# Performance work log

Hardware: AMD Instinct MI355X
Metric: run time of the kernel (lower is better)

Reference implementation:

```python
import jax, jax.numpy as jnp
import numpy as np

DIM = 128
N_HEADS = 4
HEAD_DIM = DIM // N_HEADS
K = 16
B, N = 2, 8192
BIAS_HID = 32


def knn_idx(xyz, k):
    # squared pairwise distances: [B,N,N] (same argsort order as cdist)
    sq = jnp.sum(xyz * xyz, axis=-1)  # [B,N]
    d2 = sq[:, :, None] + sq[:, None, :] - 2.0 * jnp.einsum('bnd,bmd->bnm', xyz, xyz)
    _, idx = jax.lax.top_k(-d2, k)  # smallest distances
    return idx  # [B,N,k]


def setup_inputs() -> dict:
    key = jax.random.key(0)
    ks = jax.random.split(key, 12)
    s = 1.0 / np.sqrt(DIM)
    inp = {
        'x':   jax.random.normal(ks[0], (B, N, DIM), jnp.float32),
        'xyz': jax.random.normal(ks[1], (B, N, 3), jnp.float32),
        'Wq': jax.random.uniform(ks[2], (DIM, DIM), jnp.float32, -s, s),
        'bq': jnp.zeros((DIM,), jnp.float32),
        'Wk': jax.random.uniform(ks[3], (DIM, DIM), jnp.float32, -s, s),
        'bk': jnp.zeros((DIM,), jnp.float32),
        'Wv': jax.random.uniform(ks[4], (DIM, DIM), jnp.float32, -s, s),
        'bv': jnp.zeros((DIM,), jnp.float32),
        'Wo': jax.random.uniform(ks[5], (DIM, DIM), jnp.float32, -s, s),
        'bo': jnp.zeros((DIM,), jnp.float32),
        'W1': jax.random.uniform(ks[6], (3, BIAS_HID), jnp.float32, -0.5, 0.5),
        'b1': jnp.zeros((BIAS_HID,), jnp.float32),
        'W2': jax.random.uniform(ks[7], (BIAS_HID, N_HEADS), jnp.float32, -1.0 / np.sqrt(BIAS_HID), 1.0 / np.sqrt(BIAS_HID)),
        'b2': jnp.zeros((N_HEADS,), jnp.float32),
    }
    return inp


def reference(x, xyz, Wq, bq, Wk, bk, Wv, bv, Wo, bo, W1, b1, W2, b2):
    Bb, Nn, C = x.shape
    idx = knn_idx(xyz, K)  # [B,N,k]

    q = (x @ Wq + bq).reshape(Bb, Nn, N_HEADS, HEAD_DIM)
    kf = (x @ Wk + bk).reshape(Bb, Nn, N_HEADS, HEAD_DIM)
    vf = (x @ Wv + bv).reshape(Bb, Nn, N_HEADS, HEAD_DIM)

    gather = jax.vmap(lambda f, i: f[i])  # per-batch fancy gather
    kn = gather(kf, idx)  # [B,N,k,H,D]
    vn = gather(vf, idx)  # [B,N,k,H,D]
    nxyz = gather(xyz, idx)  # [B,N,k,3]

    rel = xyz[:, :, None, :] - nxyz  # [B,N,k,3]
    bias = jax.nn.relu(rel @ W1 + b1) @ W2 + b2  # [B,N,k,H]

    scores = jnp.einsum('bnhd,bnkhd->bnhk', q, kn) / np.sqrt(HEAD_DIM)
    scores = scores + jnp.swapaxes(bias, 2, 3)  # [B,N,H,k]
    attn = jax.nn.softmax(scores, axis=-1)
    out = jnp.einsum('bnhk,bnkhd->bnhd', attn, vn).reshape(Bb, Nn, C)
    return out @ Wo + bo
```

## Files before the change

kernel.cpp:

```cpp
#include <hip/hip_runtime.h>
#include <hip/hip_bf16.h>
#include <math.h>

#define BATCH 2
#define NPT   8192
#define DIMC  128
#define NH    4
#define KNN_K 16
#define HID   32
#define BN    (BATCH*NPT)

#define TILE 1024
#define QPW  2
#define NWV  4

__device__ __forceinline__ float readlane_f(float v, int l) {
  return __int_as_float(__builtin_amdgcn_readlane(__float_as_int(v), l));
}

__global__ __launch_bounds__(256) void knn_kernel(const float* __restrict__ xyz,
                                                  int* __restrict__ knn_out) {
  __shared__ float4 spts[TILE];
  const int tid  = threadIdx.x;
  const int lane = tid & 63;
  const int wave = tid >> 6;
  const int qbase = blockIdx.x * (NWV*QPW) + wave * QPW;
  const int b = qbase / NPT;

  float qx[QPW], qy[QPW], qz[QPW], qsq[QPW];
  float topd[QPW]; int topi[QPW]; float tau[QPW];
#pragma unroll
  for (int qi = 0; qi < QPW; ++qi) {
    const int g = qbase + qi;
    qx[qi] = xyz[(size_t)g*3+0];
    qy[qi] = xyz[(size_t)g*3+1];
    qz[qi] = xyz[(size_t)g*3+2];
    qsq[qi] = __fadd_rn(__fadd_rn(__fmul_rn(qx[qi],qx[qi]),
                                  __fmul_rn(qy[qi],qy[qi])),
                        __fmul_rn(qz[qi],qz[qi]));
    topd[qi] = 3e38f; topi[qi] = 0; tau[qi] = 3e38f;
  }

  for (int t = 0; t < NPT/TILE; ++t) {
    __syncthreads();
    const float* src = xyz + (size_t)(b*NPT + t*TILE)*3;
    for (int i = tid; i < TILE; i += 256) {
      const float x = src[i*3+0], y = src[i*3+1], z = src[i*3+2];
      const float sq = __fadd_rn(__fadd_rn(__fmul_rn(x,x), __fmul_rn(y,y)),
                                 __fmul_rn(z,z));
      spts[i] = make_float4(x+x, y+y, z+z, sq);
    }
    __syncthreads();

    for (int c = 0; c < TILE/64; ++c) {
      const float4 cd = spts[c*64 + lane];
      const int cbase = t*TILE + c*64;
#pragma unroll
      for (int qi = 0; qi < QPW; ++qi) {
        float dot2 = __fadd_rn(__fadd_rn(__fmul_rn(qx[qi],cd.x),
                                         __fmul_rn(qy[qi],cd.y)),
                               __fmul_rn(qz[qi],cd.z));
        float d2 = __fsub_rn(__fadd_rn(qsq[qi], cd.w), dot2);
        unsigned long long m = __ballot(d2 < tau[qi]);
        while (m) {
          const int l = (int)__builtin_ctzll(m);
          const float dn = readlane_f(d2, l);
          const int   ni_ = cbase + l;
          const float my  = topd[qi];
          const int   myi = topi[qi];
          float ab  = __shfl_up(my, 1);
          int   abi = __shfl_up(myi, 1);
          if (lane == 0) ab = -3e38f;
          const bool ge = dn < my;
          const bool gt = dn < ab;
          topd[qi] = ge ? (gt ? ab  : dn ) : my;
          topi[qi] = ge ? (gt ? abi : ni_) : myi;
          tau[qi] = readlane_f(topd[qi], 15);
          m &= (m - 1);
          if (m) m &= __ballot(d2 < tau[qi]);
        }
      }
    }
  }

#pragma unroll
  for (int qi = 0; qi < QPW; ++qi) {
    if (lane < KNN_K) knn_out[(size_t)(qbase + qi)*KNN_K + lane] = topi[qi];
  }
}

__device__ __forceinline__ float f4c(const float4 v, int u) {
  return u == 0 ? v.x : u == 1 ? v.y : u == 2 ? v.z : v.w;
}

__global__ __launch_bounds__(256) void qkv_kernel(const float* __restrict__ x,
    const float* __restrict__ Wq, const float* __restrict__ bq,
    const float* __restrict__ Wk, const float* __restrict__ bk,
    const float* __restrict__ Wv, const float* __restrict__ bv,
    float* __restrict__ q, float* __restrict__ k, float* __restrict__ v) {
  __shared__ float xs[16*DIMC];
  const int tid = threadIdx.x;
  const int rowbase = blockIdx.x * 16;
  {
    float4* xs4 = (float4*)xs;
    const float4* src4 = (const float4*)(x + (size_t)rowbase*DIMC);
    for (int i = tid; i < 16*DIMC/4; i += 256) xs4[i] = src4[i];
  }
  __syncthreads();

  const int cg = tid & 31, rg = tid >> 5;
  const int c0 = cg * 4;
  float4 aq0 = *(const float4*)&bq[c0], aq1 = aq0;
  float4 ak0 = *(const float4*)&bk[c0], ak1 = ak0;
  float4 av0 = *(const float4*)&bv[c0], av1 = av0;

  for (int kk = 0; kk < DIMC; kk += 4) {
    const float4 xa = *(const float4*)&xs[rg*DIMC + kk];
    const float4 xb = *(const float4*)&xs[(rg+8)*DIMC + kk];
#pragma unroll
    for (int u = 0; u < 4; ++u) {
      const float4 wq = *(const float4*)&Wq[(size_t)(kk+u)*DIMC + c0];
      const float4 wk = *(const float4*)&Wk[(size_t)(kk+u)*DIMC + c0];
      const float4 wv = *(const float4*)&Wv[(size_t)(kk+u)*DIMC + c0];
      const float xau = f4c(xa, u), xbu = f4c(xb, u);
      aq0.x = fmaf(xau, wq.x, aq0.x); aq0.y = fmaf(xau, wq.y, aq0.y);
      aq0.z = fmaf(xau, wq.z, aq0.z); aq0.w = fmaf(xau, wq.w, aq0.w);
      aq1.x = fmaf(xbu, wq.x, aq1.x); aq1.y = fmaf(xbu, wq.y, aq1.y);
      aq1.z = fmaf(xbu, wq.z, aq1.z); aq1.w = fmaf(xbu, wq.w, aq1.w);
      ak0.x = fmaf(xau, wk.x, ak0.x); ak0.y = fmaf(xau, wk.y, ak0.y);
      ak0.z = fmaf(xau, wk.z, ak0.z); ak0.w = fmaf(xau, wk.w, ak0.w);
      ak1.x = fmaf(xbu, wk.x, ak1.x); ak1.y = fmaf(xbu, wk.y, ak1.y);
      ak1.z = fmaf(xbu, wk.z, ak1.z); ak1.w = fmaf(xbu, wk.w, ak1.w);
      av0.x = fmaf(xau, wv.x, av0.x); av0.y = fmaf(xau, wv.y, av0.y);
      av0.z = fmaf(xau, wv.z, av0.z); av0.w = fmaf(xau, wv.w, av0.w);
      av1.x = fmaf(xbu, wv.x, av1.x); av1.y = fmaf(xbu, wv.y, av1.y);
      av1.z = fmaf(xbu, wv.z, av1.z); av1.w = fmaf(xbu, wv.w, av1.w);
    }
  }

  const size_t r0 = (size_t)(rowbase + rg)*DIMC + c0;
  const size_t r1 = (size_t)(rowbase + rg + 8)*DIMC + c0;
  *(float4*)&q[r0] = aq0; *(float4*)&q[r1] = aq1;
  *(float4*)&k[r0] = ak0; *(float4*)&k[r1] = ak1;
  *(float4*)&v[r0] = av0; *(float4*)&v[r1] = av1;
}

template <int CTRL>
__device__ __forceinline__ float dppf(float x) {
  return __int_as_float(__builtin_amdgcn_update_dpp(
      __float_as_int(x), __float_as_int(x), CTRL, 0xF, 0xF, false));
}
#define ROR1 0x121
#define ROR2 0x122
#define ROR4 0x124
#define ROR8 0x128

__global__ __launch_bounds__(256) void attn_kernel(const float* __restrict__ xyz,
    const int* __restrict__ knn, const float* __restrict__ qb,
    const float* __restrict__ kb, const float* __restrict__ vb,
    const float* __restrict__ W1, const float* __restrict__ b1,
    const float* __restrict__ W2, const float* __restrict__ b2,
    float* __restrict__ ao) {
  __shared__ float sw[4][NH][KNN_K];
  __shared__ int   sn[4][KNN_K];
  const int tid  = threadIdx.x;
  const int wave = tid >> 6;
  const int lane = tid & 63;
  const int p = blockIdx.x * 4 + wave;
  const int b = p / NPT;
  const int h = lane >> 4;
  const int j = lane & 15;

  const int nj = knn[(size_t)p*KNN_K + j];
  if (h == 0) sn[wave][j] = nj;
  const size_t nn = (size_t)b*NPT + nj;

  const float qx0 = xyz[(size_t)p*3+0];
  const float qy0 = xyz[(size_t)p*3+1];
  const float qz0 = xyz[(size_t)p*3+2];
  const float rx = qx0 - xyz[nn*3+0];
  const float ry = qy0 - xyz[nn*3+1];
  const float rz = qz0 - xyz[nn*3+2];
  float bias = b2[h];
#pragma unroll 8
  for (int u = 0; u < HID; ++u) {
    float hv = rx*W1[0*HID+u] + ry*W1[1*HID+u] + rz*W1[2*HID+u] + b1[u];
    hv = hv > 0.f ? hv : 0.f;
    bias = fmaf(hv, W2[u*NH + h], bias);
  }

  const float* qrow = qb + (size_t)p*DIMC + h*32;
  const float* krow = kb + nn*DIMC + h*32;
  float s = 0.f;
#pragma unroll
  for (int u = 0; u < 32; u += 4) {
    const float4 qv = *(const float4*)(qrow + u);
    const float4 kv = *(const float4*)(krow + u);
    s = fmaf(qv.x, kv.x, s); s = fmaf(qv.y, kv.y, s);
    s = fmaf(qv.z, kv.z, s); s = fmaf(qv.w, kv.w, s);
  }
  s = s * 0.17677669529663689f + bias;

  float m = s;
  m = fmaxf(m, dppf<ROR1>(m));
  m = fmaxf(m, dppf<ROR2>(m));
  m = fmaxf(m, dppf<ROR4>(m));
  m = fmaxf(m, dppf<ROR8>(m));
  const float e = expf(s - m);
  float ssum = e;
  ssum += dppf<ROR1>(ssum);
  ssum += dppf<ROR2>(ssum);
  ssum += dppf<ROR4>(ssum);
  ssum += dppf<ROR8>(ssum);
  sw[wave][h][j] = e / ssum;

  __syncthreads();

  const int d0 = lane;
  const int hA = d0 >> 5;
  float out0 = 0.f, out1 = 0.f;
  const float* vbase = vb + (size_t)b*NPT*DIMC;
#pragma unroll 4
  for (int j2 = 0; j2 < KNN_K; ++j2) {
    const int n = sn[wave][j2];
    const float wA = sw[wave][hA][j2];
    const float wB = sw[wave][2+hA][j2];
    const float* vrow = vbase + (size_t)n*DIMC;
    out0 = fmaf(wA, vrow[d0],    out0);
    out1 = fmaf(wB, vrow[64+d0], out1);
  }
  ao[(size_t)p*DIMC + d0]      = out0;
  ao[(size_t)p*DIMC + 64 + d0] = out1;
}

__global__ __launch_bounds__(256) void proj_kernel(float* __restrict__ inout,
    const float* __restrict__ Wo, const float* __restrict__ bo) {
  __shared__ float xs[16*DIMC];
  const int tid = threadIdx.x;
  const int rowbase = blockIdx.x * 16;
  {
    float4* xs4 = (float4*)xs;
    const float4* src4 = (const float4*)(inout + (size_t)rowbase*DIMC);
    for (int i = tid; i < 16*DIMC/4; i += 256) xs4[i] = src4[i];
  }
  __syncthreads();

  const int cg = tid & 31, rg = tid >> 5;
  const int c0 = cg * 4;
  float4 a0 = *(const float4*)&bo[c0], a1 = a0;

  for (int kk = 0; kk < DIMC; kk += 4) {
    const float4 xa = *(const float4*)&xs[rg*DIMC + kk];
    const float4 xb = *(const float4*)&xs[(rg+8)*DIMC + kk];
#pragma unroll
    for (int u = 0; u < 4; ++u) {
      const float4 w = *(const float4*)&Wo[(size_t)(kk+u)*DIMC + c0];
      const float xau = f4c(xa, u), xbu = f4c(xb, u);
      a0.x = fmaf(xau, w.x, a0.x); a0.y = fmaf(xau, w.y, a0.y);
      a0.z = fmaf(xau, w.z, a0.z); a0.w = fmaf(xau, w.w, a0.w);
      a1.x = fmaf(xbu, w.x, a1.x); a1.y = fmaf(xbu, w.y, a1.y);
      a1.z = fmaf(xbu, w.z, a1.z); a1.w = fmaf(xbu, w.w, a1.w);
    }
  }

  *(float4*)&inout[(size_t)(rowbase + rg)*DIMC + c0]     = a0;
  *(float4*)&inout[(size_t)(rowbase + rg + 8)*DIMC + c0] = a1;
}

extern "C" void kernel_launch(void* const* d_in, const int* in_sizes, int n_in,
                              void* d_out, int out_size, void* d_ws, size_t ws_size,
                              hipStream_t stream) {
  const float* x   = (const float*)d_in[0];
  const float* xyz = (const float*)d_in[1];
  const float* Wq  = (const float*)d_in[2];
  const float* bq  = (const float*)d_in[3];
  const float* Wk  = (const float*)d_in[4];
  const float* bk  = (const float*)d_in[5];
  const float* Wv  = (const float*)d_in[6];
  const float* bv  = (const float*)d_in[7];
  const float* Wo  = (const float*)d_in[8];
  const float* bo  = (const float*)d_in[9];
  const float* W1  = (const float*)d_in[10];
  const float* b1  = (const float*)d_in[11];
  const float* W2  = (const float*)d_in[12];
  const float* b2  = (const float*)d_in[13];
  float* out = (float*)d_out;

  char* ws = (char*)d_ws;
  int*   knn = (int*)ws;
  float* q   = (float*)(ws + (size_t)(1u<<20));
  float* k   = (float*)(ws + (size_t)9*(1u<<20));
  float* v   = (float*)(ws + (size_t)17*(1u<<20));

  hipLaunchKernelGGL(knn_kernel, dim3(BN/(NWV*QPW)), dim3(256), 0, stream, xyz, knn);
  hipLaunchKernelGGL(qkv_kernel, dim3(BN/16), dim3(256), 0, stream,
                     x, Wq, bq, Wk, bk, Wv, bv, q, k, v);
  hipLaunchKernelGGL(attn_kernel, dim3(BN/4), dim3(256), 0, stream,
                     xyz, knn, q, k, v, W1, b1, W2, b2, out);
  hipLaunchKernelGGL(proj_kernel, dim3(BN/16), dim3(256), 0, stream,
                     out, Wo, bo);
}
```

Before: 206.4 us.

## Merge KNN and QKV kernels into one interleaved launch, tweak projection tiling

```diff
diff --git a/kernel.cpp b/kernel.cpp
--- a/kernel.cpp
+++ b/kernel.cpp
@@ -13,136 +13,148 @@
 #define TILE 1024
 #define QPW  2
 #define NWV  4
+#define KNNB (BN/(NWV*QPW))
+#define QKVB (BN/16)
 
 __device__ __forceinline__ float readlane_f(float v, int l) {
   return __int_as_float(__builtin_amdgcn_readlane(__float_as_int(v), l));
 }
-
-__global__ __launch_bounds__(256) void knn_kernel(const float* __restrict__ xyz,
-                                                  int* __restrict__ knn_out) {
-  __shared__ float4 spts[TILE];
-  const int tid  = threadIdx.x;
-  const int lane = tid & 63;
-  const int wave = tid >> 6;
-  const int qbase = blockIdx.x * (NWV*QPW) + wave * QPW;
-  const int b = qbase / NPT;
-
-  float qx[QPW], qy[QPW], qz[QPW], qsq[QPW];
-  float topd[QPW]; int topi[QPW]; float tau[QPW];
-#pragma unroll
-  for (int qi = 0; qi < QPW; ++qi) {
-    const int g = qbase + qi;
-    qx[qi] = xyz[(size_t)g*3+0];
-    qy[qi] = xyz[(size_t)g*3+1];
-    qz[qi] = xyz[(size_t)g*3+2];
-    qsq[qi] = __fadd_rn(__fadd_rn(__fmul_rn(qx[qi],qx[qi]),
-                                  __fmul_rn(qy[qi],qy[qi])),
-                        __fmul_rn(qz[qi],qz[qi]));
-    topd[qi] = 3e38f; topi[qi] = 0; tau[qi] = 3e38f;
-  }
-
-  for (int t = 0; t < NPT/TILE; ++t) {
-    __syncthreads();
-    const float* src = xyz + (size_t)(b*NPT + t*TILE)*3;
-    for (int i = tid; i < TILE; i += 256) {
-      const float x = src[i*3+0], y = src[i*3+1], z = src[i*3+2];
-      const float sq = __fadd_rn(__fadd_rn(__fmul_rn(x,x), __fmul_rn(y,y)),
-                                 __fmul_rn(z,z));
-      spts[i] = make_float4(x+x, y+y, z+z, sq);
-    }
-    __syncthreads();
-
-    for (int c = 0; c < TILE/64; ++c) {
-      const float4 cd = spts[c*64 + lane];
-      const int cbase = t*TILE + c*64;
-#pragma unroll
-      for (int qi = 0; qi < QPW; ++qi) {
-        float dot2 = __fadd_rn(__fadd_rn(__fmul_rn(qx[qi],cd.x),
-                                         __fmul_rn(qy[qi],cd.y)),
-                               __fmul_rn(qz[qi],cd.z));
-        float d2 = __fsub_rn(__fadd_rn(qsq[qi], cd.w), dot2);
-        unsigned long long m = __ballot(d2 < tau[qi]);
-        while (m) {
-          const int l = (int)__builtin_ctzll(m);
-          const float dn = readlane_f(d2, l);
-          const int   ni_ = cbase + l;
-          const float my  = topd[qi];
-          const int   myi = topi[qi];
-          float ab  = __shfl_up(my, 1);
-          int   abi = __shfl_up(myi, 1);
-          if (lane == 0) ab = -3e38f;
-          const bool ge = dn < my;
-          const bool gt = dn < ab;
-          topd[qi] = ge ? (gt ? ab  : dn ) : my;
-          topi[qi] = ge ? (gt ? abi : ni_) : myi;
-          tau[qi] = readlane_f(topd[qi], 15);
-          m &= (m - 1);
-          if (m) m &= __ballot(d2 < tau[qi]);
-        }
-      }
-    }
-  }
-
-#pragma unroll
-  for (int qi = 0; qi < QPW; ++qi) {
-    if (lane < KNN_K) knn_out[(size_t)(qbase + qi)*KNN_K + lane] = topi[qi];
-  }
-}
-
+__device__ __forceinline__ float dpp_shr1_f(float x) {
+  return __int_as_float(__builtin_amdgcn_update_dpp(
+      __float_as_int(x), __float_as_int(x), 0x111, 0xF, 0xF, false));
+}
+__device__ __forceinline__ int dpp_shr1_i(int x) {
+  return __builtin_amdgcn_update_dpp(x, x, 0x111, 0xF, 0xF, false);
+}
 __device__ __forceinline__ float f4c(const float4 v, int u) {
   return u == 0 ? v.x : u == 1 ? v.y : u == 2 ? v.z : v.w;
 }
 
-__global__ __launch_bounds__(256) void qkv_kernel(const float* __restrict__ x,
+__global__ __launch_bounds__(256) void knnqkv_kernel(
+    const float* __restrict__ xyz, int* __restrict__ knn_out,
+    const float* __restrict__ x,
     const float* __restrict__ Wq, const float* __restrict__ bq,
     const float* __restrict__ Wk, const float* __restrict__ bk,
     const float* __restrict__ Wv, const float* __restrict__ bv,
     float* __restrict__ q, float* __restrict__ k, float* __restrict__ v) {
-  __shared__ float xs[16*DIMC];
+  __shared__ float4 sbuf[TILE];
+  const int g   = blockIdx.x;
   const int tid = threadIdx.x;
-  const int rowbase = blockIdx.x * 16;
-  {
-    float4* xs4 = (float4*)xs;
-    const float4* src4 = (const float4*)(x + (size_t)rowbase*DIMC);
-    for (int i = tid; i < 16*DIMC/4; i += 256) xs4[i] = src4[i];
-  }
-  __syncthreads();
-
-  const int cg = tid & 31, rg = tid >> 5;
-  const int c0 = cg * 4;
-  float4 aq0 = *(const float4*)&bq[c0], aq1 = aq0;
-  float4 ak0 = *(const float4*)&bk[c0], ak1 = ak0;
-  float4 av0 = *(const float4*)&bv[c0], av1 = av0;
-
-  for (int kk = 0; kk < DIMC; kk += 4) {
-    const float4 xa = *(const float4*)&xs[rg*DIMC + kk];
-    const float4 xb = *(const float4*)&xs[(rg+8)*DIMC + kk];
-#pragma unroll
-    for (int u = 0; u < 4; ++u) {
-      const float4 wq = *(const float4*)&Wq[(size_t)(kk+u)*DIMC + c0];
-      const float4 wk = *(const float4*)&Wk[(size_t)(kk+u)*DIMC + c0];
-      const float4 wv = *(const float4*)&Wv[(size_t)(kk+u)*DIMC + c0];
-      const float xau = f4c(xa, u), xbu = f4c(xb, u);
-      aq0.x = fmaf(xau, wq.x, aq0.x); aq0.y = fmaf(xau, wq.y, aq0.y);
-      aq0.z = fmaf(xau, wq.z, aq0.z); aq0.w = fmaf(xau, wq.w, aq0.w);
-      aq1.x = fmaf(xbu, wq.x, aq1.x); aq1.y = fmaf(xbu, wq.y, aq1.y);
-      aq1.z = fmaf(xbu, wq.z, aq1.z); aq1.w = fmaf(xbu, wq.w, aq1.w);
-      ak0.x = fmaf(xau, wk.x, ak0.x); ak0.y = fmaf(xau, wk.y, ak0.y);
-      ak0.z = fmaf(xau, wk.z, ak0.z); ak0.w = fmaf(xau, wk.w, ak0.w);
-      ak1.x = fmaf(xbu, wk.x, ak1.x); ak1.y = fmaf(xbu, wk.y, ak1.y);
-      ak1.z = fmaf(xbu, wk.z, ak1.z); ak1.w = fmaf(xbu, wk.w, ak1.w);
-      av0.x = fmaf(xau, wv.x, av0.x); av0.y = fmaf(xau, wv.y, av0.y);
-      av0.z = fmaf(xau, wv.z, av0.z); av0.w = fmaf(xau, wv.w, av0.w);
-      av1.x = fmaf(xbu, wv.x, av1.x); av1.y = fmaf(xbu, wv.y, av1.y);
-      av1.z = fmaf(xbu, wv.z, av1.z); av1.w = fmaf(xbu, wv.w, av1.w);
-    }
-  }
-
-  const size_t r0 = (size_t)(rowbase + rg)*DIMC + c0;
-  const size_t r1 = (size_t)(rowbase + rg + 8)*DIMC + c0;
-  *(float4*)&q[r0] = aq0; *(float4*)&q[r1] = aq1;
-  *(float4*)&k[r0] = ak0; *(float4*)&k[r1] = ak1;
-  *(float4*)&v[r0] = av0; *(float4*)&v[r1] = av1;
+
+  if (g % 3 != 2) {
+    const int kb_  = (g/3)*2 + (g%3);
+    const int lane = tid & 63;
+    const int wave = tid >> 6;
+    const int qbase = kb_ * (NWV*QPW) + wave * QPW;
+    const int b = qbase / NPT;
+
+    float qx[QPW], qy[QPW], qz[QPW], qsq[QPW];
+    float topd[QPW]; int topi[QPW]; float tau[QPW];
+#pragma unroll
+    for (int qi = 0; qi < QPW; ++qi) {
+      const int gg = qbase + qi;
+      qx[qi] = xyz[(size_t)gg*3+0];
+      qy[qi] = xyz[(size_t)gg*3+1];
+      qz[qi] = xyz[(size_t)gg*3+2];
+      qsq[qi] = __fadd_rn(__fadd_rn(__fmul_rn(qx[qi],qx[qi]),
+                                    __fmul_rn(qy[qi],qy[qi])),
+                          __fmul_rn(qz[qi],qz[qi]));
+      topd[qi] = 3e38f; topi[qi] = 0; tau[qi] = 3e38f;
+    }
+
+    for (int t = 0; t < NPT/TILE; ++t) {
+      __syncthreads();
+      const float* src = xyz + (size_t)(b*NPT + t*TILE)*3;
+      for (int i = tid; i < TILE; i += 256) {
+        const float xx = src[i*3+0], yy = src[i*3+1], zz = src[i*3+2];
+        const float sq = __fadd_rn(__fadd_rn(__fmul_rn(xx,xx), __fmul_rn(yy,yy)),
+                                   __fmul_rn(zz,zz));
+        sbuf[i] = make_float4(xx+xx, yy+yy, zz+zz, sq);
+      }
+      __syncthreads();
+
+      for (int c = 0; c < TILE/64; ++c) {
+        const float4 cd = sbuf[c*64 + lane];
+        const int cbase = t*TILE + c*64;
+#pragma unroll
+        for (int qi = 0; qi < QPW; ++qi) {
+          float dot2 = __fadd_rn(__fadd_rn(__fmul_rn(qx[qi],cd.x),
+                                           __fmul_rn(qy[qi],cd.y)),
+                                 __fmul_rn(qz[qi],cd.z));
+          float d2 = __fsub_rn(__fadd_rn(qsq[qi], cd.w), dot2);
+          unsigned long long m = __ballot(d2 < tau[qi]);
+          while (m) {
+            const int l = (int)__builtin_ctzll(m);
+            const float dn = readlane_f(d2, l);
+            const int   ni_ = cbase + l;
+            const float my  = topd[qi];
+            const int   myi = topi[qi];
+            float ab  = dpp_shr1_f(my);
+            int   abi = dpp_shr1_i(myi);
+            if (lane == 0) ab = -3e38f;
+            const bool ge = dn < my;
+            const bool gt = dn < ab;
+            topd[qi] = ge ? (gt ? ab  : dn ) : my;
+            topi[qi] = ge ? (gt ? abi : ni_) : myi;
+            tau[qi] = readlane_f(topd[qi], 15);
+            m &= (m - 1);
+            if (m) m &= __ballot(d2 < tau[qi]);
+          }
+        }
+      }
+    }
+
+#pragma unroll
+    for (int qi = 0; qi < QPW; ++qi) {
+      if (lane < KNN_K) knn_out[(size_t)(qbase + qi)*KNN_K + lane] = topi[qi];
+    }
+  } else {
+    float* xs = (float*)sbuf;
+    const int qb_ = g/3;
+    const int rowbase = qb_ * 16;
+    {
+      float4* xs4 = (float4*)xs;
+      const float4* src4 = (const float4*)(x + (size_t)rowbase*DIMC);
+      for (int i = tid; i < 16*DIMC/4; i += 256) xs4[i] = src4[i];
+    }
+    __syncthreads();
+
+    const int cg = tid & 31, rg = tid >> 5;
+    const int c0 = cg * 4;
+    float4 aq0 = *(const float4*)&bq[c0], aq1 = aq0;
+    float4 ak0 = *(const float4*)&bk[c0], ak1 = ak0;
+    float4 av0 = *(const float4*)&bv[c0], av1 = av0;
+
+    for (int kk = 0; kk < DIMC; kk += 4) {
+      const float4 xa = *(const float4*)&xs[rg*DIMC + kk];
+      const float4 xb = *(const float4*)&xs[(rg+8)*DIMC + kk];
+#pragma unroll
+      for (int u = 0; u < 4; ++u) {
+        const float4 wq = *(const float4*)&Wq[(size_t)(kk+u)*DIMC + c0];
+        const float4 wk = *(const float4*)&Wk[(size_t)(kk+u)*DIMC + c0];
+        const float4 wv = *(const float4*)&Wv[(size_t)(kk+u)*DIMC + c0];
+        const float xau = f4c(xa, u), xbu = f4c(xb, u);
+        aq0.x = fmaf(xau, wq.x, aq0.x); aq0.y = fmaf(xau, wq.y, aq0.y);
+        aq0.z = fmaf(xau, wq.z, aq0.z); aq0.w = fmaf(xau, wq.w, aq0.w);
+        aq1.x = fmaf(xbu, wq.x, aq1.x); aq1.y = fmaf(xbu, wq.y, aq1.y);
+        aq1.z = fmaf(xbu, wq.z, aq1.z); aq1.w = fmaf(xbu, wq.w, aq1.w);
+        ak0.x = fmaf(xau, wk.x, ak0.x); ak0.y = fmaf(xau, wk.y, ak0.y);
+        ak0.z = fmaf(xau, wk.z, ak0.z); ak0.w = fmaf(xau, wk.w, ak0.w);
+        ak1.x = fmaf(xbu, wk.x, ak1.x); ak1.y = fmaf(xbu, wk.y, ak1.y);
+        ak1.z = fmaf(xbu, wk.z, ak1.z); ak1.w = fmaf(xbu, wk.w, ak1.w);
+        av0.x = fmaf(xau, wv.x, av0.x); av0.y = fmaf(xau, wv.y, av0.y);
+        av0.z = fmaf(xau, wv.z, av0.z); av0.w = fmaf(xau, wv.w, av0.w);
+        av1.x = fmaf(xbu, wv.x, av1.x); av1.y = fmaf(xbu, wv.y, av1.y);
+        av1.z = fmaf(xbu, wv.z, av1.z); av1.w = fmaf(xbu, wv.w, av1.w);
+      }
+    }
+
+    const size_t r0 = (size_t)(rowbase + rg)*DIMC + c0;
+    const size_t r1 = (size_t)(rowbase + rg + 8)*DIMC + c0;
+    *(float4*)&q[r0] = aq0; *(float4*)&q[r1] = aq1;
+    *(float4*)&k[r0] = ak0; *(float4*)&k[r1] = ak1;
+    *(float4*)&v[r0] = av0; *(float4*)&v[r1] = av1;
+  }
 }
 
 template <int CTRL>
@@ -233,38 +245,49 @@
   ao[(size_t)p*DIMC + 64 + d0] = out1;
 }
 
-__global__ __launch_bounds__(256) void proj_kernel(float* __restrict__ inout,
+#define PROJ_ROWS 16
+
+__global__ __launch_bounds__(128) void proj_kernel(float* __restrict__ inout,
     const float* __restrict__ Wo, const float* __restrict__ bo) {
-  __shared__ float xs[16*DIMC];
+  __shared__ float xs[PROJ_ROWS*DIMC];
   const int tid = threadIdx.x;
-  const int rowbase = blockIdx.x * 16;
+  const int rowbase = blockIdx.x * PROJ_ROWS;
   {
     float4* xs4 = (float4*)xs;
     const float4* src4 = (const float4*)(inout + (size_t)rowbase*DIMC);
-    for (int i = tid; i < 16*DIMC/4; i += 256) xs4[i] = src4[i];
+    for (int i = tid; i < PROJ_ROWS*DIMC/4; i += 128) xs4[i] = src4[i];
   }
   __syncthreads();
 
   const int cg = tid & 31, rg = tid >> 5;
   const int c0 = cg * 4;
-  float4 a0 = *(const float4*)&bo[c0], a1 = a0;
+  float4 a[4];
+  {
+    const float4 bo4 = *(const float4*)&bo[c0];
+#pragma unroll
+    for (int i = 0; i < 4; ++i) a[i] = bo4;
+  }
 
   for (int kk = 0; kk < DIMC; kk += 4) {
-    const float4 xa = *(const float4*)&xs[rg*DIMC + kk];
-    const float4 xb = *(const float4*)&xs[(rg+8)*DIMC + kk];
+    float4 xr[4];
+#pragma unroll
+    for (int i = 0; i < 4; ++i)
+      xr[i] = *(const float4*)&xs[(rg + 4*i)*DIMC + kk];
 #pragma unroll
     for (int u = 0; u < 4; ++u) {
       const float4 w = *(const float4*)&Wo[(size_t)(kk+u)*DIMC + c0];
-      const float xau = f4c(xa, u), xbu = f4c(xb, u);
-      a0.x = fmaf(xau, w.x, a0.x); a0.y = fmaf(xau, w.y, a0.y);
-      a0.z = fmaf(xau, w.z, a0.z); a0.w = fmaf(xau, w.w, a0.w);
-      a1.x = fmaf(xbu, w.x, a1.x); a1.y = fmaf(xbu, w.y, a1.y);
-      a1.z = fmaf(xbu, w.z, a1.z); a1.w = fmaf(xbu, w.w, a1.w);
-    }
-  }
-
-  *(float4*)&inout[(size_t)(rowbase + rg)*DIMC + c0]     = a0;
-  *(float4*)&inout[(size_t)(rowbase + rg + 8)*DIMC + c0] = a1;
+#pragma unroll
+      for (int i = 0; i < 4; ++i) {
+        const float xv = f4c(xr[i], u);
+        a[i].x = fmaf(xv, w.x, a[i].x); a[i].y = fmaf(xv, w.y, a[i].y);
+        a[i].z = fmaf(xv, w.z, a[i].z); a[i].w = fmaf(xv, w.w, a[i].w);
+      }
+    }
+  }
+
+#pragma unroll
+  for (int i = 0; i < 4; ++i)
+    *(float4*)&inout[(size_t)(rowbase + rg + 4*i)*DIMC + c0] = a[i];
 }
 
 extern "C" void kernel_launch(void* const* d_in, const int* in_sizes, int n_in,
@@ -292,11 +315,10 @@
   float* k   = (float*)(ws + (size_t)9*(1u<<20));
   float* v   = (float*)(ws + (size_t)17*(1u<<20));
 
-  hipLaunchKernelGGL(knn_kernel, dim3(BN/(NWV*QPW)), dim3(256), 0, stream, xyz, knn);
-  hipLaunchKernelGGL(qkv_kernel, dim3(BN/16), dim3(256), 0, stream,
-                     x, Wq, bq, Wk, bk, Wv, bv, q, k, v);
+  hipLaunchKernelGGL(knnqkv_kernel, dim3(KNNB + QKVB), dim3(256), 0, stream,
+                     xyz, knn, x, Wq, bq, Wk, bk, Wv, bv, q, k, v);
   hipLaunchKernelGGL(attn_kernel, dim3(BN/4), dim3(256), 0, stream,
                      xyz, knn, q, k, v, W1, b1, W2, b2, out);
-  hipLaunchKernelGGL(proj_kernel, dim3(BN/16), dim3(256), 0, stream,
+  hipLaunchKernelGGL(proj_kernel, dim3(BN/PROJ_ROWS), dim3(128), 0, stream,
                      out, Wo, bo);
 }
```

Result: faster. 188.1 us (median of 2 runs) (-8.8%).
